# Optimization experiments

Hardware: AMD Instinct MI355X
Metric: run time of the kernel (lower is better)

## Reference

```python
import jax, jax.numpy as jnp
import numpy as np

EPS = 1e-5
NUM_HEADS = 16


def rms_norm(x, w):
    v = jnp.mean(x * x, axis=-1, keepdims=True)
    return x * jax.lax.rsqrt(v + EPS) * w


def rotate_half_interleaved(x):
    # pairs (x0,x1) -> (-x1, x0), interleaved layout
    x1 = x[..., 0::2]
    x2 = x[..., 1::2]
    return jnp.stack([-x2, x1], axis=-1).reshape(x.shape)


def setup_inputs() -> dict:
    key = jax.random.key(0)
    ks = jax.random.split(key, 6)
    B, N, C = 2, 2048, 2048
    D = C // NUM_HEADS
    s = 1.0 / np.sqrt(C)
    return {
        "x": jax.random.normal(ks[0], (B, N, C), jnp.float32),
        "w_qkv": jax.random.normal(ks[1], (3 * C, C), jnp.float32) * s,
        "q_norm_w": jnp.ones((C,), jnp.float32),
        "k_norm_w": jnp.ones((C,), jnp.float32),
        "cos": jnp.cos(jax.random.normal(ks[2], (N, D), jnp.float32)),
        "sin": jnp.sin(jax.random.normal(ks[3], (N, D), jnp.float32)),
        "w_proj": jax.random.normal(ks[4], (C, C), jnp.float32) * s,
        "b_proj": jnp.zeros((C,), jnp.float32),
    }


def reference(x, w_qkv, q_norm_w, k_norm_w, cos, sin, w_proj, b_proj):
    B, N, C = x.shape
    H = NUM_HEADS
    D = C // H
    scale = D ** -0.5

    qkv = jnp.einsum("bnc,fc->bnf", x, w_qkv).reshape(B, N, 3, C)
    q, k, v = qkv[:, :, 0], qkv[:, :, 1], qkv[:, :, 2]

    # RMSNorm over full channel dim C (as in the torch module), then head split
    q = rms_norm(q, q_norm_w).reshape(B, N, H, D)
    k = rms_norm(k, k_norm_w).reshape(B, N, H, D)
    v = v.reshape(B, N, H, D)

    # rotary embedding (head_first=False layout [B,N,H,D])
    c = cos[None, :, None, :]
    s = sin[None, :, None, :]
    q = q * c + rotate_half_interleaved(q) * s
    k = k * c + rotate_half_interleaved(k) * s

    attn = jnp.einsum("bnhd,bmhd->bhnm", q, k) * scale  # [B,H,N,N]
    attn = jax.nn.softmax(attn, axis=-1)
    out = jnp.einsum("bhnm,bmhd->bnhd", attn, v).reshape(B, N, C)
    return jnp.einsum("bnc,oc->bno", out, w_proj) + b_proj
```

## Files before the change

### kernel.cpp

```cpp
#include <hip/hip_runtime.h>
#include <stdint.h>

typedef unsigned short u16;
typedef unsigned int   u32;
typedef _Float16 f16_t;
typedef f16_t f16x8 __attribute__((ext_vector_type(8)));
typedef float  f32x4  __attribute__((ext_vector_type(4)));

#define BB 2
#define NN 2048
#define CC 2048
#define HH 16
#define DD 128
#define FF 6144
#define MM 4096

__device__ __forceinline__ u16 f2h(float f){
    f16_t h = (f16_t)f;
    return __builtin_bit_cast(u16, h);
}
__device__ __forceinline__ float h2f(u16 b){
    return (float)__builtin_bit_cast(f16_t, b);
}
__device__ __forceinline__ f32x4 MFMA(f16x8 a, f16x8 b, f32x4 c){
    return __builtin_amdgcn_mfma_f32_16x16x32_f16(a, b, c, 0, 0, 0);
}
__device__ __forceinline__ void gld16(const void* g, void* l){
    __builtin_amdgcn_global_load_lds(
        (const __attribute__((address_space(1))) void*)(g),
        (__attribute__((address_space(3))) void*)(l), 16, 0, 0);
}
#define SB0() __builtin_amdgcn_sched_barrier(0)

__global__ void k_f2h3(const float* __restrict__ a0, u16* __restrict__ o0, int n0,
                       const float* __restrict__ a1, u16* __restrict__ o1, int n1,
                       const float* __restrict__ a2, u16* __restrict__ o2, int n2){
    int i = blockIdx.x * blockDim.x + threadIdx.x;
    int stride = gridDim.x * blockDim.x;
    int nt = n0 + n1 + n2;
    for (; i < nt; i += stride){
        const float4* src; ushort4* dst; int j;
        if (i < n0){ src = (const float4*)a0; dst = (ushort4*)o0; j = i; }
        else if (i < n0 + n1){ src = (const float4*)a1; dst = (ushort4*)o1; j = i - n0; }
        else { src = (const float4*)a2; dst = (ushort4*)o2; j = i - n0 - n1; }
        float4 v = src[j];
        ushort4 r; r.x = f2h(v.x); r.y = f2h(v.y); r.z = f2h(v.z); r.w = f2h(v.w);
        dst[j] = r;
    }
}

template<int OUTH>
__global__ __launch_bounds__(256) void k_gemm_bt(
    const u16* __restrict__ A, const u16* __restrict__ Bw,
    float* __restrict__ outf, u16* __restrict__ outb, u16* __restrict__ vt2o,
    const float* __restrict__ bias, int M, int N, int K)
{
    __shared__ u16 As[3][128 * 32];
    __shared__ u16 Bs[3][128 * 32];
    const int tid  = threadIdx.x;
    const int brow = blockIdx.y * 128;
    const int bcol = blockIdx.x * 128;
    const int w = tid >> 6, lane = tid & 63;
    const int wr = w >> 1, wc = w & 1;
    const int l15 = lane & 15, g = lane >> 4;
    const int sr  = tid >> 2;
    const int scz = ((tid & 3) ^ ((tid >> 3) & 3)) * 8;
    const int gx  = (g ^ ((l15 >> 1) & 3)) * 8;

    f32x4 acc[4][4];
    #pragma unroll
    for (int i = 0; i < 4; i++)
        #pragma unroll
        for (int j = 0; j < 4; j++){
            f32x4 z = {0.f, 0.f, 0.f, 0.f};
            acc[i][j] = z;
        }

    auto stage = [&](int buf, int k0){
        gld16(&Bw[(size_t)(bcol + sr) * K + k0 + scz],      &Bs[buf][w * 512]);
        gld16(&Bw[(size_t)(bcol + sr + 64) * K + k0 + scz], &Bs[buf][2048 + w * 512]);
        gld16(&A [(size_t)(brow + sr) * K + k0 + scz],      &As[buf][w * 512]);
        gld16(&A [(size_t)(brow + sr + 64) * K + k0 + scz], &As[buf][2048 + w * 512]);
    };

    stage(0, 0);
    stage(1, 32);
    int c = 0;
    for (int k0 = 0; k0 < K; k0 += 32){
        SB0();
        __builtin_amdgcn_s_barrier();
        SB0();
        int ct = c + 2; if (ct >= 3) ct -= 3;
        if (k0 + 64 < K){
            stage(ct, k0 + 64);
            asm volatile("s_waitcnt vmcnt(8)" ::: "memory");
        } else if (k0 + 32 < K){
            asm volatile("s_waitcnt vmcnt(4)" ::: "memory");
        } else {
            asm volatile("s_waitcnt vmcnt(0)" ::: "memory");
        }
        SB0();
        __builtin_amdgcn_s_barrier();
        SB0();
        f16x8 fb[4];
        #pragma unroll
        for (int j = 0; j < 4; j++){
            int row = wc * 64 + j * 16 + l15;
            fb[j] = *(const f16x8*)&Bs[c][row * 32 + gx];
        }
        #pragma unroll
        for (int i = 0; i < 4; i++){
            int row = wr * 64 + i * 16 + l15;
            f16x8 fa = *(const f16x8*)&As[c][row * 32 + gx];
            #pragma unroll
            for (int j = 0; j < 4; j++) acc[i][j] = MFMA(fa, fb[j], acc[i][j]);
        }
        c = (c + 1 == 3) ? 0 : c + 1;
    }

    if (OUTH && bcol >= 2 * CC){
        const int h  = (bcol - 2 * CC) >> 7;
        const int b  = brow >> 11;
        const int n0 = brow & (NN - 1);
        u16* vbase = vt2o + (size_t)(b * HH + h) * DD * NN;
        #pragma unroll
        for (int i = 0; i < 4; i++){
            #pragma unroll
            for (int j = 0; j < 4; j++){
                int d = wc * 64 + j * 16 + l15;
                #pragma unroll
                for (int r = 0; r < 4; r++){
                    int n = n0 + wr * 64 + i * 16 + 4 * g + r;
                    vbase[(size_t)d * NN + n] = f2h(acc[i][j][r]);
                }
            }
        }
    } else {
        #pragma unroll
        for (int i = 0; i < 4; i++){
            #pragma unroll
            for (int j = 0; j < 4; j++){
                int colg = bcol + wc * 64 + j * 16 + l15;
                #pragma unroll
                for (int r = 0; r < 4; r++){
                    int rowg = brow + wr * 64 + i * 16 + 4 * g + r;
                    float v = acc[i][j][r];
                    if (OUTH) outb[(size_t)rowg * N + colg] = f2h(v);
                    else      outf[(size_t)rowg * N + colg] = v + bias[colg];
                }
            }
        }
    }
}

__global__ __launch_bounds__(256) void k_norm_rope(
    const u16* __restrict__ qkv, const float* __restrict__ qw, const float* __restrict__ kw,
    const float* __restrict__ cosb, const float* __restrict__ sinb,
    u16* __restrict__ qout, u16* __restrict__ kout)
{
    const int m = blockIdx.x;
    const int b = m >> 11;
    const int n = m & 2047;
    const int t = threadIdx.x;
    const size_t base = (size_t)m * FF;
    const int e0 = t * 8;
    const float SCL = 0.08838834764831845f * 1.4426950408889634f;

    float qv[8], kvv[8];
    uint4 qa = *(const uint4*)&qkv[base + e0];
    uint4 ka = *(const uint4*)&qkv[base + CC + e0];
    {
        u32 aa[4] = {qa.x, qa.y, qa.z, qa.w};
        u32 bb[4] = {ka.x, ka.y, ka.z, ka.w};
        #pragma unroll
        for (int i = 0; i < 4; i++){
            qv[2*i]   = h2f((u16)(aa[i] & 0xffff));
            qv[2*i+1] = h2f((u16)(aa[i] >> 16));
            kvv[2*i]   = h2f((u16)(bb[i] & 0xffff));
            kvv[2*i+1] = h2f((u16)(bb[i] >> 16));
        }
    }
    float sq = 0.f, sk = 0.f;
    #pragma unroll
    for (int i = 0; i < 8; i++){ sq += qv[i]*qv[i]; sk += kvv[i]*kvv[i]; }
    #pragma unroll
    for (int o = 32; o > 0; o >>= 1){ sq += __shfl_xor(sq, o); sk += __shfl_xor(sk, o); }
    __shared__ float red[8];
    if ((t & 63) == 0){ red[(t >> 6)*2] = sq; red[(t >> 6)*2 + 1] = sk; }
    __syncthreads();
    sq = red[0] + red[2] + red[4] + red[6];
    sk = red[1] + red[3] + red[5] + red[7];
    const float rq = rsqrtf(sq * (1.f / 2048.f) + 1e-5f);
    const float rk = rsqrtf(sk * (1.f / 2048.f) + 1e-5f);

    const int h  = t >> 4;
    const int d0 = (t & 15) * 8;
    const float* cp = cosb + (size_t)n * DD + d0;
    const float* sp = sinb + (size_t)n * DD + d0;
    float qo[8], ko[8];
    #pragma unroll
    for (int j = 0; j < 8; j += 2){
        float c0 = cp[j], c1 = cp[j+1], s0 = sp[j], s1 = sp[j+1];
        float x0 = qv[j]   * rq * qw[e0 + j];
        float x1 = qv[j+1] * rq * qw[e0 + j + 1];
        qo[j]   = (x0 * c0 - x1 * s0) * SCL;
        qo[j+1] = (x1 * c1 + x0 * s1) * SCL;
        float y0 = kvv[j]   * rk * kw[e0 + j];
        float y1 = kvv[j+1] * rk * kw[e0 + j + 1];
        ko[j]   = y0 * c0 - y1 * s0;
        ko[j+1] = y1 * c1 + y0 * s1;
    }
    const size_t obase = ((size_t)(b * HH + h) * NN + n) * DD + d0;
    uint4 pq, pk;
    pq.x = (u32)f2h(qo[0]) | ((u32)f2h(qo[1]) << 16);
    pq.y = (u32)f2h(qo[2]) | ((u32)f2h(qo[3]) << 16);
    pq.z = (u32)f2h(qo[4]) | ((u32)f2h(qo[5]) << 16);
    pq.w = (u32)f2h(qo[6]) | ((u32)f2h(qo[7]) << 16);
    pk.x = (u32)f2h(ko[0]) | ((u32)f2h(ko[1]) << 16);
    pk.y = (u32)f2h(ko[2]) | ((u32)f2h(ko[3]) << 16);
    pk.z = (u32)f2h(ko[4]) | ((u32)f2h(ko[5]) << 16);
    pk.w = (u32)f2h(ko[6]) | ((u32)f2h(ko[7]) << 16);
    *(uint4*)&qout[obase] = pq;
    *(uint4*)&kout[obase] = pk;
}

__global__ __launch_bounds__(256, 2) void k_attn6(
    const u16* __restrict__ Q, const u16* __restrict__ Kt, const u16* __restrict__ Vt2,
    u16* __restrict__ O)
{
    __shared__ u16 Kbuf[2][8192];
    __shared__ u16 Vbuf[2][8192];
    const int tid = threadIdx.x;
    const int w = tid >> 6, lane = tid & 63;
    const int l15 = lane & 15, g = lane >> 4;
    const int flat = blockIdx.x;
    const int lid  = (flat & 7) * 64 + (flat >> 3);
    const int qb = lid & 15;
    const int h  = (lid >> 4) & 15;
    const int b  = lid >> 8;
    const size_t hb  = (size_t)(b * HH + h) * NN * DD;
    const size_t hbT = (size_t)(b * HH + h) * DD * NN;
    const int qbase = qb * 128 + w * 32;
    const int mperm = 8 * (l15 >> 2) + (l15 & 3);

    f16x8 qf[2][4];
    #pragma unroll
    for (int u = 0; u < 2; u++){
        const u16* qrow = Q + hb + (size_t)(qbase + u * 16 + l15) * DD;
        #pragma unroll
        for (int c = 0; c < 4; c++)
            qf[u][c] = *(const f16x8*)(qrow + c * 32 + 8 * g);
    }

    f32x4 oacc[2][8];
    #pragma unroll
    for (int u = 0; u < 2; u++)
        #pragma unroll
        for (int tb = 0; tb < 8; tb++){ f32x4 z = {0.f,0.f,0.f,0.f}; oacc[u][tb] = z; }
    float lsum0 = 0.f, lsum1 = 0.f;

    auto stage = [&](int buf, int kv0){
        #pragma unroll
        for (int it = 0; it < 8; it++){
            int s = it * 4 + w;
            if (s < 16){
                int hh = s >> 3, t = (s >> 2) & 1, c = s & 3;
                gld16(&Kt[hb + (size_t)(kv0 + 32 * hh + 4 * t + mperm) * DD + 32 * c + 8 * g],
                      &Kbuf[buf][s * 512]);
            } else {
                int s2 = s - 16;
                int hh = s2 >> 3, tb = s2 & 7;
                gld16(&Vt2[hbT + (size_t)(tb * 16 + l15) * NN + kv0 + 32 * hh + 8 * g],
                      &Vbuf[buf][s2 * 512]);
            }
        }
    };

    int cur = 0;
    stage(0, 0);
    for (int kv0 = 0; kv0 < NN; kv0 += 64){
        __syncthreads();
        if (kv0 + 64 < NN) stage(cur ^ 1, kv0 + 64);
        const u16* kb = &Kbuf[cur][0] + lane * 8;
        const u16* vb = &Vbuf[cur][0] + lane * 8;

        f32x4 st[2][4];
        #pragma unroll
        for (int hh = 0; hh < 2; hh++)
            #pragma unroll
            for (int q = 0; q < 4; q++){ f32x4 z = {0.f,0.f,0.f,0.f}; st[hh][q] = z; }
        __builtin_amdgcn_s_setprio(1);
        #pragma unroll
        for (int hh = 0; hh < 2; hh++){
            #pragma unroll
            for (int c = 0; c < 4; c++){
                f16x8 kf0 = *(const f16x8*)(kb + (hh * 8 + c) * 512);
                f16x8 kf1 = *(const f16x8*)(kb + (hh * 8 + 4 + c) * 512);
                st[hh][0] = MFMA(kf0, qf[0][c], st[hh][0]);
                st[hh][1] = MFMA(kf0, qf[1][c], st[hh][1]);
                st[hh][2] = MFMA(kf1, qf[0][c], st[hh][2]);
                st[hh][3] = MFMA(kf1, qf[1][c], st[hh][3]);
            }
        }
        __builtin_amdgcn_s_setprio(0);

        f16x8 pf[2][2];
        #pragma unroll
        for (int hh = 0; hh < 2; hh++){
            #pragma unroll
            for (int r = 0; r < 4; r++){
                float e00 = exp2f(st[hh][0][r]), e10 = exp2f(st[hh][2][r]);
                float e01 = exp2f(st[hh][1][r]), e11 = exp2f(st[hh][3][r]);
                lsum0 += e00 + e10;
                lsum1 += e01 + e11;
                pf[hh][0][r] = (f16_t)e00; pf[hh][0][r + 4] = (f16_t)e10;
                pf[hh][1][r] = (f16_t)e01; pf[hh][1][r + 4] = (f16_t)e11;
            }
        }

        __builtin_amdgcn_s_setprio(1);
        #pragma unroll
        for (int hh = 0; hh < 2; hh++){
            #pragma unroll
            for (int tb = 0; tb < 8; tb++){
                f16x8 vf = *(const f16x8*)(vb + (hh * 8 + tb) * 512);
                oacc[0][tb] = MFMA(pf[hh][0], vf, oacc[0][tb]);
                oacc[1][tb] = MFMA(pf[hh][1], vf, oacc[1][tb]);
            }
        }
        __builtin_amdgcn_s_setprio(0);
        cur ^= 1;
    }

    lsum0 += __shfl_xor(lsum0, 16); lsum0 += __shfl_xor(lsum0, 32);
    lsum1 += __shfl_xor(lsum1, 16); lsum1 += __shfl_xor(lsum1, 32);
    float linv0 = 1.f / lsum0, linv1 = 1.f / lsum1;
    float li0[4], li1[4];
    #pragma unroll
    for (int r = 0; r < 4; r++){
        li0[r] = __shfl(linv0, 4 * g + r);
        li1[r] = __shfl(linv1, 4 * g + r);
    }

    #pragma unroll
    for (int tb = 0; tb < 8; tb++){
        #pragma unroll
        for (int r = 0; r < 4; r++){
            int q0 = qbase + 4 * g + r;
            O[(size_t)(b * NN + q0) * CC + h * DD + tb * 16 + l15] = f2h(oacc[0][tb][r] * li0[r]);
            int q1 = qbase + 16 + 4 * g + r;
            O[(size_t)(b * NN + q1) * CC + h * DD + tb * 16 + l15] = f2h(oacc[1][tb][r] * li1[r]);
        }
    }
}

extern "C" void kernel_launch(void* const* d_in, const int* in_sizes, int n_in,
                              void* d_out, int out_size, void* d_ws, size_t ws_size,
                              hipStream_t stream) {
    const float* x      = (const float*)d_in[0];
    const float* w_qkv  = (const float*)d_in[1];
    const float* qw     = (const float*)d_in[2];
    const float* kw     = (const float*)d_in[3];
    const float* cosb   = (const float*)d_in[4];
    const float* sinb   = (const float*)d_in[5];
    const float* w_proj = (const float*)d_in[6];
    const float* b_proj = (const float*)d_in[7];
    float* out = (float*)d_out;

    const size_t sz_xh   = (size_t)MM * CC * 2;
    const size_t sz_wqkv = (size_t)FF * CC * 2;
    const size_t sz_wprj = (size_t)CC * CC * 2;
    const size_t sz_qkv  = (size_t)MM * FF * 2;
    const size_t sz_t    = (size_t)BB * HH * NN * DD * 2;
    const size_t need = sz_xh + sz_wqkv + sz_wprj + sz_qkv + sz_t*3 + sz_xh;
    if (ws_size < need) return;

    char* ws = (char*)d_ws;
    size_t off = 0;
    auto alloc = [&](size_t bytes){ void* p = ws + off; off += (bytes + 255) & ~(size_t)255; return p; };
    u16* x_h     = (u16*)alloc(sz_xh);
    u16* wqkv_h  = (u16*)alloc(sz_wqkv);
    u16* wprj_h  = (u16*)alloc(sz_wprj);
    u16* qkv     = (u16*)alloc(sz_qkv);
    u16* qr      = (u16*)alloc(sz_t);
    u16* kr      = (u16*)alloc(sz_t);
    u16* vt2     = (u16*)alloc(sz_t);
    u16* ob      = (u16*)alloc(sz_xh);

    k_f2h3<<<2048, 256, 0, stream>>>(x, x_h, MM * CC / 4,
                                     w_qkv, wqkv_h, FF * CC / 4,
                                     w_proj, wprj_h, CC * CC / 4);
    k_gemm_bt<1><<<dim3(FF / 128, MM / 128), 256, 0, stream>>>(
        x_h, wqkv_h, nullptr, qkv, vt2, nullptr, MM, FF, CC);
    k_norm_rope<<<MM, 256, 0, stream>>>(qkv, qw, kw, cosb, sinb, qr, kr);
    k_attn6<<<512, 256, 0, stream>>>(qr, kr, vt2, ob);
    k_gemm_bt<0><<<dim3(CC / 128, MM / 128), 256, 0, stream>>>(
        ob, wprj_h, out, nullptr, nullptr, b_proj, MM, CC, CC);
}
```

Baseline: 305.7 us.

## Pre-swizzle x into MFMA fragment layout and load A directly to registers

The fp32-to-fp16 conversion kernel now writes x in a fragment-tiled layout matching the 16x32 MFMA A-operand order and converts 8 elements per thread. The QKV GEMM reads A fragments straight from global memory into registers (double-buffered), staging only B through LDS, with explicit vmcnt waits. This removes A's LDS staging and reads, cutting LDS traffic and footprint. The trade-off is that A is no longer shared in LDS, so each A tile is fetched from global once per wave column (twice per block) instead of once per block.

```diff
diff --git a/kernel.cpp b/kernel.cpp
--- a/kernel.cpp
+++ b/kernel.cpp
@@ -32,28 +32,154 @@
 }
 #define SB0() __builtin_amdgcn_sched_barrier(0)
 
-__global__ void k_f2h3(const float* __restrict__ a0, u16* __restrict__ o0, int n0,
-                       const float* __restrict__ a1, u16* __restrict__ o1, int n1,
-                       const float* __restrict__ a2, u16* __restrict__ o2, int n2){
+__global__ void k_f2h3(const float* __restrict__ x,  u16* __restrict__ xf,
+                       const float* __restrict__ w1, u16* __restrict__ o1, int n1,
+                       const float* __restrict__ w2, u16* __restrict__ o2, int n2){
+    const int nx = MM * CC / 8;
     int i = blockIdx.x * blockDim.x + threadIdx.x;
     int stride = gridDim.x * blockDim.x;
-    int nt = n0 + n1 + n2;
+    int nt = nx + n1 + n2;
     for (; i < nt; i += stride){
-        const float4* src; ushort4* dst; int j;
-        if (i < n0){ src = (const float4*)a0; dst = (ushort4*)o0; j = i; }
-        else if (i < n0 + n1){ src = (const float4*)a1; dst = (ushort4*)o1; j = i - n0; }
-        else { src = (const float4*)a2; dst = (ushort4*)o2; j = i - n0 - n1; }
-        float4 v = src[j];
-        ushort4 r; r.x = f2h(v.x); r.y = f2h(v.y); r.z = f2h(v.z); r.w = f2h(v.w);
-        dst[j] = r;
-    }
-}
-
-template<int OUTH>
-__global__ __launch_bounds__(256) void k_gemm_bt(
+        float4 v0, v1; u16* dst;
+        if (i < nx){
+            int lane = i & 63, kblk = (i >> 6) & 63, rt = i >> 12;
+            int row = rt * 16 + (lane & 15);
+            int col = kblk * 32 + (lane >> 4) * 8;
+            const float4* s = (const float4*)(x + (size_t)row * CC + col);
+            v0 = s[0]; v1 = s[1];
+            dst = xf + (size_t)i * 8;
+        } else if (i < nx + n1){
+            int j = i - nx;
+            const float4* s = (const float4*)w1 + (size_t)j * 2;
+            v0 = s[0]; v1 = s[1];
+            dst = o1 + (size_t)j * 8;
+        } else {
+            int j = i - nx - n1;
+            const float4* s = (const float4*)w2 + (size_t)j * 2;
+            v0 = s[0]; v1 = s[1];
+            dst = o2 + (size_t)j * 8;
+        }
+        u16 o[8] = {f2h(v0.x), f2h(v0.y), f2h(v0.z), f2h(v0.w),
+                    f2h(v1.x), f2h(v1.y), f2h(v1.z), f2h(v1.w)};
+        *(uint4*)dst = *(uint4*)o;
+    }
+}
+
+__global__ __launch_bounds__(256) void k_gemm_qkv(
+    const u16* __restrict__ Axf, const u16* __restrict__ Bw,
+    u16* __restrict__ outb, u16* __restrict__ vt2o, int M, int N, int K)
+{
+    __shared__ u16 Bs[3][128 * 32];
+    const int tid  = threadIdx.x;
+    const int brow = blockIdx.y * 128;
+    const int bcol = blockIdx.x * 128;
+    const int w = tid >> 6, lane = tid & 63;
+    const int wr = w >> 1, wc = w & 1;
+    const int l15 = lane & 15, g = lane >> 4;
+    const int sr  = tid >> 2;
+    const int scz = ((tid & 3) ^ ((tid >> 3) & 3)) * 8;
+    const int gx  = (g ^ ((l15 >> 1) & 3)) * 8;
+    const int KB  = K >> 5;
+    const size_t rt0 = (size_t)(brow >> 4) + wr * 4;
+
+    f32x4 acc[4][4];
+    #pragma unroll
+    for (int i = 0; i < 4; i++)
+        #pragma unroll
+        for (int j = 0; j < 4; j++){
+            f32x4 z = {0.f, 0.f, 0.f, 0.f};
+            acc[i][j] = z;
+        }
+
+    auto stageB = [&](int buf, int k0){
+        gld16(&Bw[(size_t)(bcol + sr) * K + k0 + scz],      &Bs[buf][w * 512]);
+        gld16(&Bw[(size_t)(bcol + sr + 64) * K + k0 + scz], &Bs[buf][2048 + w * 512]);
+    };
+    auto loadA = [&](int k0, f16x8 (&af)[4]){
+        int kblk = k0 >> 5;
+        #pragma unroll
+        for (int i = 0; i < 4; i++)
+            af[i] = *(const f16x8*)(Axf + (((rt0 + i) * KB + kblk) * 64 + lane) * 8);
+    };
+    auto compute = [&](int buf, const f16x8 (&af)[4]){
+        f16x8 fb[4];
+        #pragma unroll
+        for (int j = 0; j < 4; j++){
+            int row = wc * 64 + j * 16 + l15;
+            fb[j] = *(const f16x8*)&Bs[buf][row * 32 + gx];
+        }
+        #pragma unroll
+        for (int i = 0; i < 4; i++)
+            #pragma unroll
+            for (int j = 0; j < 4; j++) acc[i][j] = MFMA(af[i], fb[j], acc[i][j]);
+    };
+
+    f16x8 afa[4], afb[4];
+    stageB(0, 0);
+    stageB(1, 32);
+    loadA(0, afa);
+    int c = 0;
+    const int nK = KB;
+    for (int t = 0; t < nK; t += 2){
+        SB0(); __builtin_amdgcn_s_barrier(); SB0();
+        int ct = c + 2; if (ct >= 3) ct -= 3;
+        if (t + 2 < nK) stageB(ct, (t + 2) * 32);
+        loadA((t + 1) * 32, afb);
+        SB0();
+        if (t + 2 < nK) asm volatile("s_waitcnt vmcnt(6)" ::: "memory");
+        else            asm volatile("s_waitcnt vmcnt(4)" ::: "memory");
+        SB0(); __builtin_amdgcn_s_barrier(); SB0();
+        compute(c, afa);
+        c = (c + 1 == 3) ? 0 : c + 1;
+        SB0(); __builtin_amdgcn_s_barrier(); SB0();
+        ct = c + 2; if (ct >= 3) ct -= 3;
+        if (t + 3 < nK) stageB(ct, (t + 3) * 32);
+        if (t + 2 < nK) loadA((t + 2) * 32, afa);
+        SB0();
+        if (t + 3 < nK)      asm volatile("s_waitcnt vmcnt(6)" ::: "memory");
+        else if (t + 2 < nK) asm volatile("s_waitcnt vmcnt(4)" ::: "memory");
+        else                 asm volatile("s_waitcnt vmcnt(0)" ::: "memory");
+        SB0(); __builtin_amdgcn_s_barrier(); SB0();
+        compute(c, afb);
+        c = (c + 1 == 3) ? 0 : c + 1;
+    }
+
+    if (bcol >= 2 * CC){
+        const int h  = (bcol - 2 * CC) >> 7;
+        const int b  = brow >> 11;
+        const int n0 = brow & (NN - 1);
+        u16* vbase = vt2o + (size_t)(b * HH + h) * DD * NN;
+        #pragma unroll
+        for (int i = 0; i < 4; i++){
+            #pragma unroll
+            for (int j = 0; j < 4; j++){
+                int d = wc * 64 + j * 16 + l15;
+                #pragma unroll
+                for (int r = 0; r < 4; r++){
+                    int n = n0 + wr * 64 + i * 16 + 4 * g + r;
+                    vbase[(size_t)d * NN + n] = f2h(acc[i][j][r]);
+                }
+            }
+        }
+    } else {
+        #pragma unroll
+        for (int i = 0; i < 4; i++){
+            #pragma unroll
+            for (int j = 0; j < 4; j++){
+                int colg = bcol + wc * 64 + j * 16 + l15;
+                #pragma unroll
+                for (int r = 0; r < 4; r++){
+                    int rowg = brow + wr * 64 + i * 16 + 4 * g + r;
+                    outb[(size_t)rowg * N + colg] = f2h(acc[i][j][r]);
+                }
+            }
+        }
+    }
+}
+
+__global__ __launch_bounds__(256) void k_gemm_proj(
     const u16* __restrict__ A, const u16* __restrict__ Bw,
-    float* __restrict__ outf, u16* __restrict__ outb, u16* __restrict__ vt2o,
-    const float* __restrict__ bias, int M, int N, int K)
+    float* __restrict__ outf, const float* __restrict__ bias, int M, int N, int K)
 {
     __shared__ u16 As[3][128 * 32];
     __shared__ u16 Bs[3][128 * 32];
@@ -118,36 +244,15 @@
         c = (c + 1 == 3) ? 0 : c + 1;
     }
 
-    if (OUTH && bcol >= 2 * CC){
-        const int h  = (bcol - 2 * CC) >> 7;
-        const int b  = brow >> 11;
-        const int n0 = brow & (NN - 1);
-        u16* vbase = vt2o + (size_t)(b * HH + h) * DD * NN;
-        #pragma unroll
-        for (int i = 0; i < 4; i++){
-            #pragma unroll
-            for (int j = 0; j < 4; j++){
-                int d = wc * 64 + j * 16 + l15;
-                #pragma unroll
-                for (int r = 0; r < 4; r++){
-                    int n = n0 + wr * 64 + i * 16 + 4 * g + r;
-                    vbase[(size_t)d * NN + n] = f2h(acc[i][j][r]);
-                }
-            }
-        }
-    } else {
-        #pragma unroll
-        for (int i = 0; i < 4; i++){
-            #pragma unroll
-            for (int j = 0; j < 4; j++){
-                int colg = bcol + wc * 64 + j * 16 + l15;
-                #pragma unroll
-                for (int r = 0; r < 4; r++){
-                    int rowg = brow + wr * 64 + i * 16 + 4 * g + r;
-                    float v = acc[i][j][r];
-                    if (OUTH) outb[(size_t)rowg * N + colg] = f2h(v);
-                    else      outf[(size_t)rowg * N + colg] = v + bias[colg];
-                }
+    #pragma unroll
+    for (int i = 0; i < 4; i++){
+        #pragma unroll
+        for (int j = 0; j < 4; j++){
+            int colg = bcol + wc * 64 + j * 16 + l15;
+            #pragma unroll
+            for (int r = 0; r < 4; r++){
+                int rowg = brow + wr * 64 + i * 16 + 4 * g + r;
+                outf[(size_t)rowg * N + colg] = acc[i][j][r] + bias[colg];
             }
         }
     }
@@ -378,7 +483,7 @@
     char* ws = (char*)d_ws;
     size_t off = 0;
     auto alloc = [&](size_t bytes){ void* p = ws + off; off += (bytes + 255) & ~(size_t)255; return p; };
-    u16* x_h     = (u16*)alloc(sz_xh);
+    u16* xf      = (u16*)alloc(sz_xh);
     u16* wqkv_h  = (u16*)alloc(sz_wqkv);
     u16* wprj_h  = (u16*)alloc(sz_wprj);
     u16* qkv     = (u16*)alloc(sz_qkv);
@@ -387,13 +492,13 @@
     u16* vt2     = (u16*)alloc(sz_t);
     u16* ob      = (u16*)alloc(sz_xh);
 
-    k_f2h3<<<2048, 256, 0, stream>>>(x, x_h, MM * CC / 4,
-                                     w_qkv, wqkv_h, FF * CC / 4,
-                                     w_proj, wprj_h, CC * CC / 4);
-    k_gemm_bt<1><<<dim3(FF / 128, MM / 128), 256, 0, stream>>>(
-        x_h, wqkv_h, nullptr, qkv, vt2, nullptr, MM, FF, CC);
+    k_f2h3<<<2048, 256, 0, stream>>>(x, xf,
+                                     w_qkv, wqkv_h, FF * CC / 8,
+                                     w_proj, wprj_h, CC * CC / 8);
+    k_gemm_qkv<<<dim3(FF / 128, MM / 128), 256, 0, stream>>>(
+        xf, wqkv_h, qkv, vt2, MM, FF, CC);
     k_norm_rope<<<MM, 256, 0, stream>>>(qkv, qw, kw, cosb, sinb, qr, kr);
     k_attn6<<<512, 256, 0, stream>>>(qr, kr, vt2, ob);
-    k_gemm_bt<0><<<dim3(CC / 128, MM / 128), 256, 0, stream>>>(
-        ob, wprj_h, out, nullptr, nullptr, b_proj, MM, CC, CC);
-}
+    k_gemm_proj<<<dim3(CC / 128, MM / 128), 256, 0, stream>>>(
+        ob, wprj_h, out, b_proj, MM, CC, CC);
+}
```

Result: slower. 316.6 us (+3.6%).
